# Kernel tuning notes

Hardware: AMD Instinct MI355X
Metric: run time of the kernel (lower is better)

Reference implementation:

```python
import jax, jax.numpy as jnp
import numpy as np

ACCEL_LIMIT = 1.0
OMEGA_LIMIT = 1.0
B, N_IN, H1, H21, H22 = 32768, 8, 2048, 1024, 1024
N_CL = 2


def setup_inputs() -> dict:
    key = jax.random.key(0)
    ks = jax.random.split(key, 16)
    def g(k, shape, scale):
        return (jax.random.normal(k, shape, dtype=jnp.float32) * scale)
    inp = {
        "x": jax.random.normal(ks[0], (B, N_IN), dtype=jnp.float32),
        "W1": g(ks[1], (N_IN, H1), (2.0 / N_IN) ** 0.5),
        "b1": jnp.zeros((H1,), jnp.float32),
        "W21": g(ks[2], (H1, H21), (2.0 / H1) ** 0.5),
        "b21": jnp.zeros((H21,), jnp.float32),
        "W31": g(ks[3], (H21, N_CL), (1.0 / H21) ** 0.5),
        "b31": jnp.zeros((N_CL,), jnp.float32),
        "W22": g(ks[4], (H1, H22), (2.0 / H1) ** 0.5),
        "b22": jnp.zeros((H22,), jnp.float32),
        "W32": g(ks[5], (H22, N_CL), (1.0 / H22) ** 0.5),
        "b32": jnp.zeros((N_CL,), jnp.float32),
        "input_mean": jax.random.normal(ks[6], (N_IN,), dtype=jnp.float32),
        "input_std": jax.random.uniform(ks[7], (N_IN,), jnp.float32, 0.5, 1.5),
        "output_mean": jax.random.normal(ks[8], (N_CL,), dtype=jnp.float32) * 0.1,
        "output_std": jax.random.uniform(ks[9], (N_CL,), jnp.float32, 0.5, 1.5),
        "s0": jnp.ones((1,), jnp.float32),
        "s1": jnp.ones((1,), jnp.float32),
        "s2": jnp.ones((1,), jnp.float32),
        "s3": jnp.ones((1,), jnp.float32),
        "sgn": 1,
    }
    return inp


def reference(x, W1, b1, W21, b21, W31, b31, W22, b22, W32, b32,
              input_mean, input_std, output_mean, output_std,
              s0, s1, s2, s3, sgn):
    # De-normalized raw state (used by disabled liveness branch; kept for fidelity)
    x0 = x * input_std + input_mean  # [B, N_IN]
    h = jax.nn.relu(x @ W1 + b1)                 # [B, H1]
    x31 = jax.nn.relu(h @ W21 + b21) @ W31 + b31  # reference control, [B, 2]
    x32 = 4.0 * jax.nn.sigmoid(jax.nn.relu(h @ W22 + b22) @ W32 + b32)  # HOCBF penalties (unused in limits-only QP)
    x31_actual = x31 * output_std + output_mean   # [B, 2]

    # QP: min 0.5 u^T I u + x31_actual^T u  s.t. box constraints from control limits.
    # G rows: [0,1]<=a+s0, [0,-1]<=a+s1, [1,0]<=w+s2, [-1,0]<=w+s3.
    # Q=I and axis-aligned constraints -> closed form: u = clip(-p, lower, upper).
    upper = jnp.concatenate([OMEGA_LIMIT + s2, ACCEL_LIMIT + s0])   # [2]
    lower = jnp.concatenate([-(OMEGA_LIMIT + s3), -(ACCEL_LIMIT + s1)])  # [2]
    u = jnp.minimum(jnp.maximum(-x31_actual, lower), upper)         # [B, 2]

    out = (u - output_mean) / output_std
    return out
```

## Files before the change

kernel.cpp:

```cpp
#include <hip/hip_runtime.h>
#include <hip/hip_bf16.h>
#include <hip/hip_fp16.h>

#define DEVI __device__ __forceinline__

typedef _Float16 f16x8 __attribute__((ext_vector_type(8)));
typedef float f32x4 __attribute__((ext_vector_type(4)));

static constexpr int M = 32768;
static constexpr int N = 1024;
static constexpr int K = 2048;
static constexpr int BM = 256, BN = 256, BK = 64;
static constexpr int NT = K / BK;
static constexpr int NSTRIP = (N / BN) * 4;

static constexpr size_t WS_H    = 0;
static constexpr size_t WS_W21T = 134217728;
static constexpr size_t WS_PART = 134217728 + 4194304;

using lds_vp = __attribute__((address_space(3))) void*;
using gbl_vp = const __attribute__((address_space(1))) void*;

DEVI void async_ld16(const void* g, void* l) {
  __builtin_amdgcn_global_load_lds((gbl_vp)(size_t)g,
                                   (lds_vp)(uint32_t)(size_t)l,
                                   16, 0, 0);
}

__global__ __launch_bounds__(256)
void w21cvt_kernel(const float* __restrict__ W21, _Float16* __restrict__ w21t) {
  __shared__ float sT[64][65];
  const int tid = threadIdx.x;
  const int k0 = blockIdx.x * 64;
  const int n0 = blockIdx.y * 64;
  const int row = tid >> 2;
#pragma unroll
  for (int q = 0; q < 4; ++q) {
    int c = (tid & 3) * 4 + q * 16;
    float4 v = *(const float4*)(W21 + (size_t)(k0 + row) * 1024 + n0 + c);
    sT[row][c + 0] = v.x; sT[row][c + 1] = v.y;
    sT[row][c + 2] = v.z; sT[row][c + 3] = v.w;
  }
  __syncthreads();
  const int n  = tid >> 2;
  const int kc = (tid & 3) * 16;
  union { _Float16 h[16]; float4 f4[2]; } u;
#pragma unroll
  for (int e = 0; e < 16; ++e) u.h[e] = (_Float16)sT[kc + e][n];
  float4* dst = (float4*)(w21t + (size_t)(n0 + n) * 2048 + k0 + kc);
  dst[0] = u.f4[0]; dst[1] = u.f4[1];
}

__global__ __launch_bounds__(256)
void gemm1_kernel(const float* __restrict__ x, const float* __restrict__ W1,
                  const float* __restrict__ b1, _Float16* __restrict__ hout) {
  __shared__ float sx[64 * 8];
  const int tid = threadIdx.x;
  const int r0 = blockIdx.x * 64;
  if (tid < 128) {
    *(float4*)&sx[tid * 4] = *(const float4*)(x + (size_t)r0 * 8 + tid * 4);
  }
  float w1r[8][8];
#pragma unroll
  for (int j = 0; j < 8; ++j) {
    *(float4*)&w1r[j][0] = *(const float4*)(W1 + j * 2048 + tid * 8);
    *(float4*)&w1r[j][4] = *(const float4*)(W1 + j * 2048 + tid * 8 + 4);
  }
  float bb[8];
  *(float4*)&bb[0] = *(const float4*)(b1 + tid * 8);
  *(float4*)&bb[4] = *(const float4*)(b1 + tid * 8 + 4);
  __syncthreads();
  for (int r = 0; r < 64; ++r) {
    float xv[8];
    *(float4*)&xv[0] = *(float4*)&sx[r * 8];
    *(float4*)&xv[4] = *(float4*)&sx[r * 8 + 4];
    float acc[8];
#pragma unroll
    for (int c = 0; c < 8; ++c) acc[c] = bb[c];
#pragma unroll
    for (int j = 0; j < 8; ++j)
#pragma unroll
      for (int c = 0; c < 8; ++c) acc[c] = fmaf(xv[j], w1r[j][c], acc[c]);
    union { f16x8 v; float4 f4; } u;
#pragma unroll
    for (int c = 0; c < 8; ++c) u.v[c] = (_Float16)fmaxf(acc[c], 0.f);
    *(float4*)(hout + (size_t)(r0 + r) * 2048 + tid * 8) = u.f4;
  }
}

__global__ __launch_bounds__(512, 2)
void gemm2_kernel(const _Float16* __restrict__ h, const _Float16* __restrict__ w21t,
                  const float* __restrict__ b21, const float* __restrict__ w31,
                  float* __restrict__ part) {
  __shared__ __align__(16) char smem[131072];

  const int tid  = threadIdx.x;
  const int lane = tid & 63;
  const int w    = tid >> 6;
  const int wr   = w >> 2;
  const int wc   = w & 3;

  const int lin  = blockIdx.x;
  const int swz  = (lin & 7) * 64 + (lin >> 3);
  const int nblk = swz & 3;
  const int mblk = swz >> 2;
  const int r0 = mblk * BM;
  const int n0 = nblk * BN;

  f32x4 acc[8][4] = {};

  const int cA = ((tid & 3) - (tid >> 3)) & 3;
  const _Float16* pA = h    + (size_t)(r0 + (tid >> 2)) * K + cA * 8;
  const _Float16* pB = w21t + (size_t)(n0 + (tid >> 2)) * K + cA * 8;
  char* const lbase = smem + tid * 16;

  auto stageA = [&](int t, int hs) {
    const _Float16* g = pA + t * 64 + hs * 32;
    char* l = lbase + (t & 1) * 65536 + hs * 16384;
    async_ld16(g,                     l);
    async_ld16(g + (size_t)128 * K,   l + 8192);
  };
  auto stageB = [&](int t, int hs) {
    const _Float16* g = pB + t * 64 + hs * 32;
    char* l = lbase + (t & 1) * 65536 + 32768 + hs * 16384;
    async_ld16(g,                     l);
    async_ld16(g + (size_t)128 * K,   l + 8192);
  };

  const int arow0 = wr * 128 + (lane & 15);
  const int aslot = ((lane >> 4) + (arow0 >> 1)) & 3;
  const int abyte = arow0 * 64 + aslot * 16;
  const int brow0 = wc * 64 + (lane & 15);
  const int bslot = ((lane >> 4) + (brow0 >> 1)) & 3;
  const int bbyte = 32768 + brow0 * 64 + bslot * 16;

  stageB(0, 0); stageA(0, 0); stageB(0, 1); stageA(0, 1);
  stageB(1, 0); stageA(1, 0); stageB(1, 1);
  asm volatile("s_waitcnt vmcnt(10)" ::: "memory");
  __builtin_amdgcn_s_barrier();

  for (int t = 0; t < NT; ++t) {
    const char* base = smem + (t & 1) * 65536;
    f16x8 aF[4], bF[4];

#pragma unroll
    for (int m = 0; m < 4; ++m) aF[m] = *(const f16x8*)(base + abyte + m * 1024);
#pragma unroll
    for (int n = 0; n < 4; ++n) bF[n] = *(const f16x8*)(base + bbyte + n * 1024);
    if (t + 1 < NT) stageA(t + 1, 1);
    __builtin_amdgcn_s_barrier();
    asm volatile("s_waitcnt lgkmcnt(0)" ::: "memory");
    __builtin_amdgcn_sched_barrier(0);
    __builtin_amdgcn_s_setprio(1);
#pragma unroll
    for (int m = 0; m < 4; ++m)
#pragma unroll
      for (int n = 0; n < 4; ++n)
        acc[m][n] = __builtin_amdgcn_mfma_f32_16x16x32_f16(aF[m], bF[n], acc[m][n], 0, 0, 0);
    __builtin_amdgcn_s_setprio(0);
    __builtin_amdgcn_sched_barrier(0);
    __builtin_amdgcn_s_barrier();

#pragma unroll
    for (int m = 0; m < 4; ++m) aF[m] = *(const f16x8*)(base + abyte + (m + 4) * 1024);
    if (t + 2 < NT) stageB(t + 2, 0);
    if (t < NT - 2) asm volatile("s_waitcnt vmcnt(10)" ::: "memory");
    else            asm volatile("s_waitcnt vmcnt(0)"  ::: "memory");
    __builtin_amdgcn_s_barrier();
    asm volatile("s_waitcnt lgkmcnt(0)" ::: "memory");
    __builtin_amdgcn_sched_barrier(0);
    __builtin_amdgcn_s_setprio(1);
#pragma unroll
    for (int m = 0; m < 4; ++m)
#pragma unroll
      for (int n = 0; n < 4; ++n)
        acc[m + 4][n] = __builtin_amdgcn_mfma_f32_16x16x32_f16(aF[m], bF[n], acc[m + 4][n], 0, 0, 0);
    __builtin_amdgcn_s_setprio(0);
    __builtin_amdgcn_sched_barrier(0);
    __builtin_amdgcn_s_barrier();

#pragma unroll
    for (int m = 0; m < 4; ++m) aF[m] = *(const f16x8*)(base + 16384 + abyte + m * 1024);
#pragma unroll
    for (int n = 0; n < 4; ++n) bF[n] = *(const f16x8*)(base + 16384 + bbyte + n * 1024);
    if (t + 2 < NT) stageA(t + 2, 0);
    __builtin_amdgcn_s_barrier();
    asm volatile("s_waitcnt lgkmcnt(0)" ::: "memory");
    __builtin_amdgcn_sched_barrier(0);
    __builtin_amdgcn_s_setprio(1);
#pragma unroll
    for (int m = 0; m < 4; ++m)
#pragma unroll
      for (int n = 0; n < 4; ++n)
        acc[m][n] = __builtin_amdgcn_mfma_f32_16x16x32_f16(aF[m], bF[n], acc[m][n], 0, 0, 0);
    __builtin_amdgcn_s_setprio(0);
    __builtin_amdgcn_sched_barrier(0);
    __builtin_amdgcn_s_barrier();

#pragma unroll
    for (int m = 0; m < 4; ++m) aF[m] = *(const f16x8*)(base + 16384 + abyte + (m + 4) * 1024);
    if (t + 2 < NT) stageB(t + 2, 1);
    if (t < NT - 2) asm volatile("s_waitcnt vmcnt(10)" ::: "memory");
    else            asm volatile("s_waitcnt vmcnt(0)"  ::: "memory");
    __builtin_amdgcn_s_barrier();
    asm volatile("s_waitcnt lgkmcnt(0)" ::: "memory");
    __builtin_amdgcn_sched_barrier(0);
    __builtin_amdgcn_s_setprio(1);
#pragma unroll
    for (int m = 0; m < 4; ++m)
#pragma unroll
      for (int n = 0; n < 4; ++n)
        acc[m + 4][n] = __builtin_amdgcn_mfma_f32_16x16x32_f16(aF[m], bF[n], acc[m + 4][n], 0, 0, 0);
    __builtin_amdgcn_s_setprio(0);
    __builtin_amdgcn_sched_barrier(0);
    __builtin_amdgcn_s_barrier();
  }

  float bb[4], w0v[4], w1v[4];
#pragma unroll
  for (int n = 0; n < 4; ++n) {
    int cg = n0 + wc * 64 + n * 16 + (lane & 15);
    bb[n]  = b21[cg];
    w0v[n] = w31[cg * 2 + 0];
    w1v[n] = w31[cg * 2 + 1];
  }
  float* red = (float*)smem;
#pragma unroll
  for (int m = 0; m < 8; ++m) {
#pragma unroll
    for (int j = 0; j < 4; ++j) {
      float s0 = 0.f, s1 = 0.f;
#pragma unroll
      for (int n = 0; n < 4; ++n) {
        float a = fmaxf(acc[m][n][j] + bb[n], 0.f);
        s0 = fmaf(a, w0v[n], s0);
        s1 = fmaf(a, w1v[n], s1);
      }
      int row_local = m * 16 + (lane >> 4) * 4 + j;
      int idx = w * 4096 + row_local * 32 + (lane & 15) * 2;
      red[idx]     = s0;
      red[idx + 1] = s1;
    }
  }
  __syncthreads();
#pragma unroll
  for (int q = tid; q < 1024; q += 512) {
    const int w2 = q >> 7, rl = q & 127;
    const float* src = red + w2 * 4096 + rl * 32;
    float a0 = 0.f, a1 = 0.f;
#pragma unroll
    for (int k = 0; k < 8; ++k) {
      int kk = (k + (tid & 7)) & 7;
      float4 v = *(const float4*)(src + kk * 4);
      a0 += v.x + v.z;
      a1 += v.y + v.w;
    }
    int gr = r0 + (w2 >> 2) * 128 + rl;
    int strip = nblk * 4 + (w2 & 3);
    float2 o; o.x = a0; o.y = a1;
    *(float2*)(part + ((size_t)strip * M + gr) * 2) = o;
  }
}

__global__ __launch_bounds__(256)
void final_kernel(const float* __restrict__ part, const float* __restrict__ b31,
                  const float* __restrict__ om, const float* __restrict__ os,
                  const float* __restrict__ s0p, const float* __restrict__ s1p,
                  const float* __restrict__ s2p, const float* __restrict__ s3p,
                  float* __restrict__ out) {
  const int r = blockIdx.x * blockDim.x + threadIdx.x;
  float a0 = b31[0], a1 = b31[1];
#pragma unroll
  for (int s = 0; s < NSTRIP; ++s) {
    float2 v = *(const float2*)(part + ((size_t)s * M + r) * 2);
    a0 += v.x; a1 += v.y;
  }
  const float om0 = om[0], om1 = om[1], os0 = os[0], os1 = os[1];
  const float xa0 = a0 * os0 + om0;
  const float xa1 = a1 * os1 + om1;
  const float up0 = 1.0f + s2p[0];
  const float up1 = 1.0f + s0p[0];
  const float lo0 = -(1.0f + s3p[0]);
  const float lo1 = -(1.0f + s1p[0]);
  const float u0 = fminf(fmaxf(-xa0, lo0), up0);
  const float u1 = fminf(fmaxf(-xa1, lo1), up1);
  float2 o; o.x = (u0 - om0) / os0; o.y = (u1 - om1) / os1;
  *(float2*)(out + (size_t)r * 2) = o;
}

extern "C" void kernel_launch(void* const* d_in, const int* in_sizes, int n_in,
                              void* d_out, int out_size, void* d_ws, size_t ws_size,
                              hipStream_t stream) {
  const float* x    = (const float*)d_in[0];
  const float* W1   = (const float*)d_in[1];
  const float* b1   = (const float*)d_in[2];
  const float* W21  = (const float*)d_in[3];
  const float* b21  = (const float*)d_in[4];
  const float* W31  = (const float*)d_in[5];
  const float* b31  = (const float*)d_in[6];
  const float* omean = (const float*)d_in[13];
  const float* ostd  = (const float*)d_in[14];
  const float* s0 = (const float*)d_in[15];
  const float* s1 = (const float*)d_in[16];
  const float* s2 = (const float*)d_in[17];
  const float* s3 = (const float*)d_in[18];
  float* out = (float*)d_out;

  char* ws = (char*)d_ws;
  _Float16* hbuf = (_Float16*)(ws + WS_H);
  _Float16* w21t = (_Float16*)(ws + WS_W21T);
  float*    part = (float*)(ws + WS_PART);

  w21cvt_kernel<<<dim3(32, 16), dim3(256), 0, stream>>>(W21, w21t);
  gemm1_kernel<<<dim3(512), dim3(256), 0, stream>>>(x, W1, b1, hbuf);
  gemm2_kernel<<<dim3((M / BM) * (N / BN)), dim3(512), 0, stream>>>(hbuf, w21t, b21, W31, part);
  final_kernel<<<dim3(M / 256), dim3(256), 0, stream>>>(part, b31, omean, ostd,
                                                        s0, s1, s2, s3, out);
}
```

Measured before the change: 152.3 us.

## Double-buffer LDS fragment reads in registers to overlap with MFMA phases

Restructures the GEMM main loop so LDS-to-register fragment reads for the next MFMA phase are issued before the current phase's MFMAs, using ping-pong register sets (ar0/ar1, br0/br1) and partial lgkmcnt waits instead of waiting for all reads. The last K-tile is peeled into an epilogue. The aim is to hide LDS read latency behind matrix-core work. In exchange it raises VGPR pressure, which could lower occupancy or cause spills, and the partial waitcnt counts must exactly match the number of outstanding reads.

```diff
diff --git a/kernel.cpp b/kernel.cpp
--- a/kernel.cpp
+++ b/kernel.cpp
@@ -134,86 +134,110 @@
   const int bslot = ((lane >> 4) + (brow0 >> 1)) & 3;
   const int bbyte = 32768 + brow0 * 64 + bslot * 16;
 
+  auto rdA4 = [&](f16x8* d, const char* basep, int sh, int mlo) {
+#pragma unroll
+    for (int m = 0; m < 4; ++m)
+      d[m] = *(const f16x8*)(basep + sh * 16384 + abyte + (mlo + m) * 1024);
+  };
+  auto rdB4 = [&](f16x8* d, const char* basep, int sh) {
+#pragma unroll
+    for (int n = 0; n < 4; ++n)
+      d[n] = *(const f16x8*)(basep + sh * 16384 + bbyte + n * 1024);
+  };
+  auto mm = [&](const f16x8* a, const f16x8* b, int moff) {
+#pragma unroll
+    for (int m = 0; m < 4; ++m)
+#pragma unroll
+      for (int n = 0; n < 4; ++n)
+        acc[m + moff][n] =
+            __builtin_amdgcn_mfma_f32_16x16x32_f16(a[m], b[n], acc[m + moff][n], 0, 0, 0);
+  };
+
+#define SB __builtin_amdgcn_sched_barrier(0)
+#define BAR __builtin_amdgcn_s_barrier()
+#define LGKM(nn) asm volatile("s_waitcnt lgkmcnt(" #nn ")" ::: "memory")
+
+  f16x8 ar0[4], ar1[4], br0[4], br1[4];
+
   stageB(0, 0); stageA(0, 0); stageB(0, 1); stageA(0, 1);
   stageB(1, 0); stageA(1, 0); stageB(1, 1);
   asm volatile("s_waitcnt vmcnt(10)" ::: "memory");
-  __builtin_amdgcn_s_barrier();
-
-  for (int t = 0; t < NT; ++t) {
-    const char* base = smem + (t & 1) * 65536;
-    f16x8 aF[4], bF[4];
-
-#pragma unroll
-    for (int m = 0; m < 4; ++m) aF[m] = *(const f16x8*)(base + abyte + m * 1024);
-#pragma unroll
-    for (int n = 0; n < 4; ++n) bF[n] = *(const f16x8*)(base + bbyte + n * 1024);
-    if (t + 1 < NT) stageA(t + 1, 1);
-    __builtin_amdgcn_s_barrier();
-    asm volatile("s_waitcnt lgkmcnt(0)" ::: "memory");
-    __builtin_amdgcn_sched_barrier(0);
+  BAR;
+  {
+    const char* b0 = smem;
+    rdA4(ar0, b0, 0, 0);
+    rdB4(br0, b0, 0);
+  }
+
+  for (int t = 0; t < NT - 1; ++t) {
+    const char* base  = smem + (t & 1) * 65536;
+    const char* baseN = smem + ((t + 1) & 1) * 65536;
+
+    rdA4(ar1, base, 0, 4);
+    stageA(t + 1, 1);
+    SB;
+    BAR; LGKM(4); SB;
     __builtin_amdgcn_s_setprio(1);
-#pragma unroll
-    for (int m = 0; m < 4; ++m)
-#pragma unroll
-      for (int n = 0; n < 4; ++n)
-        acc[m][n] = __builtin_amdgcn_mfma_f32_16x16x32_f16(aF[m], bF[n], acc[m][n], 0, 0, 0);
-    __builtin_amdgcn_s_setprio(0);
-    __builtin_amdgcn_sched_barrier(0);
-    __builtin_amdgcn_s_barrier();
-
-#pragma unroll
-    for (int m = 0; m < 4; ++m) aF[m] = *(const f16x8*)(base + abyte + (m + 4) * 1024);
+    mm(ar0, br0, 0);
+    __builtin_amdgcn_s_setprio(0); SB;
+    BAR;
+
     if (t + 2 < NT) stageB(t + 2, 0);
     if (t < NT - 2) asm volatile("s_waitcnt vmcnt(10)" ::: "memory");
     else            asm volatile("s_waitcnt vmcnt(0)"  ::: "memory");
-    __builtin_amdgcn_s_barrier();
-    asm volatile("s_waitcnt lgkmcnt(0)" ::: "memory");
-    __builtin_amdgcn_sched_barrier(0);
+    rdA4(ar0, base, 1, 0);
+    rdB4(br1, base, 1);
+    SB;
+    BAR; LGKM(8); SB;
     __builtin_amdgcn_s_setprio(1);
-#pragma unroll
-    for (int m = 0; m < 4; ++m)
-#pragma unroll
-      for (int n = 0; n < 4; ++n)
-        acc[m + 4][n] = __builtin_amdgcn_mfma_f32_16x16x32_f16(aF[m], bF[n], acc[m + 4][n], 0, 0, 0);
-    __builtin_amdgcn_s_setprio(0);
-    __builtin_amdgcn_sched_barrier(0);
-    __builtin_amdgcn_s_barrier();
-
-#pragma unroll
-    for (int m = 0; m < 4; ++m) aF[m] = *(const f16x8*)(base + 16384 + abyte + m * 1024);
-#pragma unroll
-    for (int n = 0; n < 4; ++n) bF[n] = *(const f16x8*)(base + 16384 + bbyte + n * 1024);
+    mm(ar1, br0, 4);
+    __builtin_amdgcn_s_setprio(0); SB;
+    BAR;
+
+    rdA4(ar1, base, 1, 4);
     if (t + 2 < NT) stageA(t + 2, 0);
-    __builtin_amdgcn_s_barrier();
-    asm volatile("s_waitcnt lgkmcnt(0)" ::: "memory");
-    __builtin_amdgcn_sched_barrier(0);
+    SB;
+    BAR; LGKM(4); SB;
     __builtin_amdgcn_s_setprio(1);
-#pragma unroll
-    for (int m = 0; m < 4; ++m)
-#pragma unroll
-      for (int n = 0; n < 4; ++n)
-        acc[m][n] = __builtin_amdgcn_mfma_f32_16x16x32_f16(aF[m], bF[n], acc[m][n], 0, 0, 0);
-    __builtin_amdgcn_s_setprio(0);
-    __builtin_amdgcn_sched_barrier(0);
-    __builtin_amdgcn_s_barrier();
-
-#pragma unroll
-    for (int m = 0; m < 4; ++m) aF[m] = *(const f16x8*)(base + 16384 + abyte + (m + 4) * 1024);
+    mm(ar0, br1, 0);
+    __builtin_amdgcn_s_setprio(0); SB;
+    BAR;
+
     if (t + 2 < NT) stageB(t + 2, 1);
     if (t < NT - 2) asm volatile("s_waitcnt vmcnt(10)" ::: "memory");
     else            asm volatile("s_waitcnt vmcnt(0)"  ::: "memory");
-    __builtin_amdgcn_s_barrier();
-    asm volatile("s_waitcnt lgkmcnt(0)" ::: "memory");
-    __builtin_amdgcn_sched_barrier(0);
+    rdA4(ar0, baseN, 0, 0);
+    rdB4(br0, baseN, 0);
+    SB;
+    BAR; LGKM(8); SB;
     __builtin_amdgcn_s_setprio(1);
-#pragma unroll
-    for (int m = 0; m < 4; ++m)
-#pragma unroll
-      for (int n = 0; n < 4; ++n)
-        acc[m + 4][n] = __builtin_amdgcn_mfma_f32_16x16x32_f16(aF[m], bF[n], acc[m + 4][n], 0, 0, 0);
-    __builtin_amdgcn_s_setprio(0);
-    __builtin_amdgcn_sched_barrier(0);
-    __builtin_amdgcn_s_barrier();
+    mm(ar1, br1, 4);
+    __builtin_amdgcn_s_setprio(0); SB;
+    BAR;
+  }
+
+  {
+    const char* base = smem + ((NT - 1) & 1) * 65536;
+
+    rdA4(ar1, base, 0, 4);
+    SB; BAR; LGKM(4); SB;
+    __builtin_amdgcn_s_setprio(1); mm(ar0, br0, 0); __builtin_amdgcn_s_setprio(0); SB;
+    BAR;
+
+    rdA4(ar0, base, 1, 0);
+    rdB4(br1, base, 1);
+    SB; BAR; LGKM(8); SB;
+    __builtin_amdgcn_s_setprio(1); mm(ar1, br0, 4); __builtin_amdgcn_s_setprio(0); SB;
+    BAR;
+
+    rdA4(ar1, base, 1, 4);
+    SB; BAR; LGKM(4); SB;
+    __builtin_amdgcn_s_setprio(1); mm(ar0, br1, 0); __builtin_amdgcn_s_setprio(0); SB;
+    BAR;
+
+    LGKM(0); SB;
+    __builtin_amdgcn_s_setprio(1); mm(ar1, br1, 4); __builtin_amdgcn_s_setprio(0); SB;
+    BAR;
   }
 
   float bb[4], w0v[4], w1v[4];
@@ -260,6 +284,9 @@
     float2 o; o.x = a0; o.y = a1;
     *(float2*)(part + ((size_t)strip * M + gr) * 2) = o;
   }
+#undef SB
+#undef BAR
+#undef LGKM
 }
 
 __global__ __launch_bounds__(256)
```

After: 151.8 us. About the same (-0.4%).

## Restructure GEMM main loop into two half-tile phases with full-tile prefetch

Applied to the files above, without the earlier changes.

Reorganises the K-loop of the fused GEMM from four quarter phases to two half-K phases. Each phase loads all 8 A fragments and 4 B fragments at once and issues 32 MFMAs. Global-to-LDS prefetch for tile t+2 is now issued as whole A+B halves after the barrier, and the vmcnt wait happens once per iteration. The aim is fewer barriers and waitcnt stalls per tile. In exchange, register pressure rises from holding 8 A fragments, and the prefetch now has a different amount of overlap with the LDS reads.

```diff
diff --git a/kernel.cpp b/kernel.cpp
--- a/kernel.cpp
+++ b/kernel.cpp
@@ -134,86 +134,54 @@
   const int bslot = ((lane >> 4) + (brow0 >> 1)) & 3;
   const int bbyte = 32768 + brow0 * 64 + bslot * 16;
 
-  stageB(0, 0); stageA(0, 0); stageB(0, 1); stageA(0, 1);
-  stageB(1, 0); stageA(1, 0); stageB(1, 1);
-  asm volatile("s_waitcnt vmcnt(10)" ::: "memory");
-  __builtin_amdgcn_s_barrier();
+#define SB __builtin_amdgcn_sched_barrier(0)
+#define BAR __builtin_amdgcn_s_barrier()
+#define LGKM0 asm volatile("s_waitcnt lgkmcnt(0)" ::: "memory")
+
+  stageA(0, 0); stageB(0, 0); stageA(0, 1); stageB(0, 1);
+  stageA(1, 0); stageB(1, 0); stageA(1, 1); stageB(1, 1);
+  asm volatile("s_waitcnt vmcnt(8)" ::: "memory");
+  BAR;
 
   for (int t = 0; t < NT; ++t) {
     const char* base = smem + (t & 1) * 65536;
-    f16x8 aF[4], bF[4];
-
-#pragma unroll
-    for (int m = 0; m < 4; ++m) aF[m] = *(const f16x8*)(base + abyte + m * 1024);
+    f16x8 aF[8], bF[4];
+
+#pragma unroll
+    for (int m = 0; m < 8; ++m) aF[m] = *(const f16x8*)(base + abyte + m * 1024);
 #pragma unroll
     for (int n = 0; n < 4; ++n) bF[n] = *(const f16x8*)(base + bbyte + n * 1024);
-    if (t + 1 < NT) stageA(t + 1, 1);
-    __builtin_amdgcn_s_barrier();
-    asm volatile("s_waitcnt lgkmcnt(0)" ::: "memory");
-    __builtin_amdgcn_sched_barrier(0);
+    SB;
+    BAR; LGKM0; SB;
+    if (t + 2 < NT) { stageA(t + 2, 0); stageB(t + 2, 0); }
+    SB;
     __builtin_amdgcn_s_setprio(1);
 #pragma unroll
-    for (int m = 0; m < 4; ++m)
+    for (int m = 0; m < 8; ++m)
 #pragma unroll
       for (int n = 0; n < 4; ++n)
         acc[m][n] = __builtin_amdgcn_mfma_f32_16x16x32_f16(aF[m], bF[n], acc[m][n], 0, 0, 0);
-    __builtin_amdgcn_s_setprio(0);
-    __builtin_amdgcn_sched_barrier(0);
-    __builtin_amdgcn_s_barrier();
-
-#pragma unroll
-    for (int m = 0; m < 4; ++m) aF[m] = *(const f16x8*)(base + abyte + (m + 4) * 1024);
-    if (t + 2 < NT) stageB(t + 2, 0);
-    if (t < NT - 2) asm volatile("s_waitcnt vmcnt(10)" ::: "memory");
-    else            asm volatile("s_waitcnt vmcnt(0)"  ::: "memory");
-    __builtin_amdgcn_s_barrier();
-    asm volatile("s_waitcnt lgkmcnt(0)" ::: "memory");
-    __builtin_amdgcn_sched_barrier(0);
+    __builtin_amdgcn_s_setprio(0); SB;
+    BAR;
+
+#pragma unroll
+    for (int m = 0; m < 8; ++m) aF[m] = *(const f16x8*)(base + 16384 + abyte + m * 1024);
+#pragma unroll
+    for (int n = 0; n < 4; ++n) bF[n] = *(const f16x8*)(base + 16384 + bbyte + n * 1024);
+    SB;
+    BAR; LGKM0; SB;
+    if (t + 2 < NT) { stageA(t + 2, 1); stageB(t + 2, 1); }
+    SB;
     __builtin_amdgcn_s_setprio(1);
 #pragma unroll
-    for (int m = 0; m < 4; ++m)
-#pragma unroll
-      for (int n = 0; n < 4; ++n)
-        acc[m + 4][n] = __builtin_amdgcn_mfma_f32_16x16x32_f16(aF[m], bF[n], acc[m + 4][n], 0, 0, 0);
-    __builtin_amdgcn_s_setprio(0);
-    __builtin_amdgcn_sched_barrier(0);
-    __builtin_amdgcn_s_barrier();
-
-#pragma unroll
-    for (int m = 0; m < 4; ++m) aF[m] = *(const f16x8*)(base + 16384 + abyte + m * 1024);
-#pragma unroll
-    for (int n = 0; n < 4; ++n) bF[n] = *(const f16x8*)(base + 16384 + bbyte + n * 1024);
-    if (t + 2 < NT) stageA(t + 2, 0);
-    __builtin_amdgcn_s_barrier();
-    asm volatile("s_waitcnt lgkmcnt(0)" ::: "memory");
-    __builtin_amdgcn_sched_barrier(0);
-    __builtin_amdgcn_s_setprio(1);
-#pragma unroll
-    for (int m = 0; m < 4; ++m)
+    for (int m = 0; m < 8; ++m)
 #pragma unroll
       for (int n = 0; n < 4; ++n)
         acc[m][n] = __builtin_amdgcn_mfma_f32_16x16x32_f16(aF[m], bF[n], acc[m][n], 0, 0, 0);
-    __builtin_amdgcn_s_setprio(0);
-    __builtin_amdgcn_sched_barrier(0);
-    __builtin_amdgcn_s_barrier();
-
-#pragma unroll
-    for (int m = 0; m < 4; ++m) aF[m] = *(const f16x8*)(base + 16384 + abyte + (m + 4) * 1024);
-    if (t + 2 < NT) stageB(t + 2, 1);
-    if (t < NT - 2) asm volatile("s_waitcnt vmcnt(10)" ::: "memory");
-    else            asm volatile("s_waitcnt vmcnt(0)"  ::: "memory");
-    __builtin_amdgcn_s_barrier();
-    asm volatile("s_waitcnt lgkmcnt(0)" ::: "memory");
-    __builtin_amdgcn_sched_barrier(0);
-    __builtin_amdgcn_s_setprio(1);
-#pragma unroll
-    for (int m = 0; m < 4; ++m)
-#pragma unroll
-      for (int n = 0; n < 4; ++n)
-        acc[m + 4][n] = __builtin_amdgcn_mfma_f32_16x16x32_f16(aF[m], bF[n], acc[m + 4][n], 0, 0, 0);
-    __builtin_amdgcn_s_setprio(0);
-    __builtin_amdgcn_sched_barrier(0);
-    __builtin_amdgcn_s_barrier();
+    __builtin_amdgcn_s_setprio(0); SB;
+    if (t < NT - 2) asm volatile("s_waitcnt vmcnt(8)" ::: "memory");
+    else            asm volatile("s_waitcnt vmcnt(0)" ::: "memory");
+    BAR;
   }
 
   float bb[4], w0v[4], w1v[4];
@@ -260,6 +228,9 @@
     float2 o; o.x = a0; o.y = a1;
     *(float2*)(part + ((size_t)strip * M + gr) * 2) = o;
   }
+#undef SB
+#undef BAR
+#undef LGKM0
 }
 
 __global__ __launch_bounds__(256)
```

Measured after the change: 155.6 us. 2.2% more time.
